# Kernel tuning notes

Measured on AMD Instinct MI355X. Metric: run time of the kernel, lower is better.

The kernel has to match this reference:

```python
import jax, jax.numpy as jnp
import numpy as np

N_NODES = 100000
N_EDGES = 1600000
FEATS = 128
HIDDEN = 64
N_CLASS = 40
NEG_SLOPE = 0.01  # torch leaky_relu default


def _glorot(key, shape):
    lim = float(np.sqrt(6.0 / (shape[0] + shape[1])))
    return jax.random.uniform(key, shape, jnp.float32, -lim, lim)


def setup_inputs() -> dict:
    key = jax.random.key(0)
    ks = jax.random.split(key, 10)
    x = jax.random.normal(ks[0], (N_NODES, FEATS), jnp.float32)
    edge_index = jax.random.randint(ks[1], (2, N_EDGES), 0, N_NODES, jnp.int64)
    edge_weight = jax.random.uniform(ks[2], (N_EDGES,), jnp.float32)
    return {
        "x": x,
        "edge_index": edge_index,
        "edge_weight": edge_weight,
        "W_first": _glorot(ks[3], (FEATS, HIDDEN)),
        "b_first": jnp.zeros((HIDDEN,), jnp.float32),
        "Wc1": _glorot(ks[4], (HIDDEN, HIDDEN)),
        "bc1": jnp.zeros((HIDDEN,), jnp.float32),
        "Wc2": _glorot(ks[5], (HIDDEN, HIDDEN)),
        "bc2": jnp.zeros((HIDDEN,), jnp.float32),
        "W_out": _glorot(ks[6], (HIDDEN, N_CLASS)),
        "b_out": jnp.zeros((N_CLASS,), jnp.float32),
    }


def _gcn_norm(edge_index, edge_weight, n):
    # PyG gcn_norm with add_self_loops=True: A_hat = D^-1/2 (A + I) D^-1/2
    loop = jnp.arange(n, dtype=edge_index.dtype)
    src = jnp.concatenate([edge_index[0], loop])
    dst = jnp.concatenate([edge_index[1], loop])
    ew = jnp.concatenate([edge_weight, jnp.ones((n,), edge_weight.dtype)])
    deg = jax.ops.segment_sum(ew, dst, num_segments=n)  # degree at target
    dis = jnp.where(deg > 0, jax.lax.rsqrt(deg), 0.0)
    norm = dis[src] * ew * dis[dst]  # [E+N]
    return src, dst, norm


def _gcn_conv(h, src, dst, norm, W, b, n):
    h = h @ W                                   # [N, H]
    msg = norm[:, None] * h[src]                # gather + scale  [E+N, H]
    out = jax.ops.segment_sum(msg, dst, num_segments=n)  # scatter-add
    return out + b


def reference(x, edge_index, edge_weight, W_first, b_first, Wc1, bc1, Wc2, bc2, W_out, b_out):
    n = x.shape[0]
    src, dst, norm = _gcn_norm(edge_index, edge_weight, n)
    h = jax.nn.leaky_relu(x @ W_first + b_first, NEG_SLOPE)
    # dropout is identity in eval mode
    h = jax.nn.leaky_relu(_gcn_conv(h, src, dst, norm, Wc1, bc1, n), NEG_SLOPE)
    h = jax.nn.leaky_relu(_gcn_conv(h, src, dst, norm, Wc2, bc2, n), NEG_SLOPE)
    logits = h @ W_out + b_out
    return jax.nn.log_softmax(logits, axis=-1)
```

## Files before the change

kernel.cpp:

```cpp
#include <hip/hip_runtime.h>
#include <hip/hip_bf16.h>
#include <math.h>

#define NFEATS 128
#define NHID   64
#define NCLS   40
#define NEG_SLOPE 0.01f

#define GSH_S  9
#define GSPAN_S 512
#define GCAP_S 9216
#define SB     2048

typedef float f32x4 __attribute__((ext_vector_type(4)));
typedef int   i32x2 __attribute__((ext_vector_type(2)));

__device__ inline unsigned short f2bfu(float v) {
    union { float f; unsigned int u; } x; x.f = v;
    unsigned int r = (x.u + 0x7FFFu + ((x.u >> 16) & 1u)) >> 16;
    return (unsigned short)r;
}
__device__ inline float bf2f(unsigned short u) {
    union { unsigned int u32; float f; } x; x.u32 = ((unsigned int)u) << 16;
    return x.f;
}
__device__ inline float bflo(unsigned int u) {
    union { unsigned int v; float f; } x; x.v = u << 16; return x.f;
}
__device__ inline float bfhi(unsigned int u) {
    union { unsigned int v; float f; } x; x.v = u & 0xFFFF0000u; return x.f;
}

__device__ inline void role_split(int i, int nA, int nB, int* ia, int* ib) {
    *ia = -1; *ib = -1;
    int m2 = 2 * min(nA, nB);
    if (i < m2) { if (i & 1) *ib = i >> 1; else *ia = i >> 1; }
    else if (nA > nB) *ia = i - nB;
    else *ib = i - nA;
}


__global__ __launch_bounds__(256) void stage_gemm1_kernel(
    const int* __restrict__ srcA, const int* __restrict__ dstA, const float* __restrict__ ew,
    int* __restrict__ gcur, int2* __restrict__ staged, int E, int nStage, int ngrp,
    const float* __restrict__ x, const float* __restrict__ W1, const float* __restrict__ b1,
    float* __restrict__ h1, int n, int nTile) {
    __shared__ __align__(16) float Ws[64 * 64];

    int ia, ib;
    role_split(blockIdx.x, nStage, nTile, &ia, &ib);
    int tid = threadIdx.x;

    if (ia >= 0) {
        int* hist = (int*)Ws;
        int* wcur = ((int*)Ws) + 256;
        if (tid < 256) hist[tid] = 0;
        __syncthreads();

        int q0 = (ia * SB) >> 2;
        int qend = min(q0 + SB / 4, E >> 2);
        int dcache[8], scache[8];
        float wcache[8];

#pragma unroll
        for (int it = 0; it < 2; ++it) {
            int q = q0 + it * 256 + tid;
            bool ok = (q < qend);
            int4 d4 = ok ? ((const int4*)dstA)[q] : make_int4(-1, -1, -1, -1);
            int4 s4 = ok ? ((const int4*)srcA)[q] : make_int4(0, 0, 0, 0);
            float4 w4 = ok ? ((const float4*)ew)[q] : make_float4(0, 0, 0, 0);
            dcache[it * 4 + 0] = d4.x; dcache[it * 4 + 1] = d4.y;
            dcache[it * 4 + 2] = d4.z; dcache[it * 4 + 3] = d4.w;
            scache[it * 4 + 0] = s4.x; scache[it * 4 + 1] = s4.y;
            scache[it * 4 + 2] = s4.z; scache[it * 4 + 3] = s4.w;
            wcache[it * 4 + 0] = w4.x; wcache[it * 4 + 1] = w4.y;
            wcache[it * 4 + 2] = w4.z; wcache[it * 4 + 3] = w4.w;
#pragma unroll
            for (int j = 0; j < 4; ++j)
                if (dcache[it * 4 + j] >= 0) atomicAdd(&hist[dcache[it * 4 + j] >> GSH_S], 1);
        }
        if (ia == nStage - 1) {
            for (int e = (E & ~3) + tid; e < E; e += 256) atomicAdd(&hist[dstA[e] >> GSH_S], 1);
        }
        __syncthreads();

        if (tid < ngrp) {
            int c = hist[tid];
            wcur[tid] = (c > 0) ? atomicAdd(&gcur[tid], c) : 0;
        }
        __syncthreads();

        int pos[8];
#pragma unroll
        for (int j = 0; j < 8; ++j) {
            int d = dcache[j];
            pos[j] = (d >= 0) ? atomicAdd(&wcur[d >> GSH_S], 1) : GCAP_S;
        }
#pragma unroll
        for (int j = 0; j < 8; ++j) {
            int d = dcache[j];
            if (d >= 0 && pos[j] < GCAP_S)
                staged[(size_t)(d >> GSH_S) * GCAP_S + pos[j]] =
                    make_int2(((d & (GSPAN_S - 1)) << 17) | scache[j], __float_as_int(wcache[j]));
        }
        if (ia == nStage - 1) {
            for (int e = (E & ~3) + tid; e < E; e += 256) {
                int d = dstA[e];
                int g = d >> GSH_S;
                int p = atomicAdd(&wcur[g], 1);
                if (p < GCAP_S)
                    staged[(size_t)g * GCAP_S + p] =
                        make_int2(((d & (GSPAN_S - 1)) << 17) | srcA[e], __float_as_int(ew[e]));
            }
        }
        return;
    }

    int c4 = (tid & 15) * 4;
    int r0 = ib * 64 + (tid >> 4) * 4;
    int rr[4];
#pragma unroll
    for (int i = 0; i < 4; ++i) rr[i] = min(r0 + i, n - 1);

    float acc[4][4] = {};
    for (int ph = 0; ph < 2; ++ph) {
        __syncthreads();
        for (int i = tid; i < 64 * 16; i += 256)
            ((float4*)Ws)[i] = ((const float4*)W1)[ph * 1024 + i];
        __syncthreads();
#pragma unroll 2
        for (int kk = 0; kk < 64; kk += 4) {
            f32x4 av[4], bv[4];
#pragma unroll
            for (int i = 0; i < 4; ++i)
                av[i] = __builtin_nontemporal_load(
                    (const f32x4*)&x[(size_t)rr[i] * NFEATS + ph * 64 + kk]);
#pragma unroll
            for (int q = 0; q < 4; ++q) bv[q] = *(const f32x4*)&Ws[(kk + q) * 64 + c4];
#pragma unroll
            for (int i = 0; i < 4; ++i) {
#pragma unroll
                for (int q = 0; q < 4; ++q) {
                    float a = av[i][q];
#pragma unroll
                    for (int j = 0; j < 4; ++j) acc[i][j] += a * bv[q][j];
                }
            }
        }
    }

#pragma unroll
    for (int i = 0; i < 4; ++i) {
        int rw = r0 + i;
        if (rw >= n) break;
        float4 o;
        float* oa = (float*)&o;
#pragma unroll
        for (int j = 0; j < 4; ++j) {
            float v = acc[i][j] + b1[c4 + j];
            oa[j] = (v > 0.0f) ? v : v * NEG_SLOPE;
        }
        *(float4*)&h1[(size_t)rw * 64 + c4] = o;
    }
}


__global__ __launch_bounds__(512) void degsort_kernel(
    const int* __restrict__ gcur, const int2* __restrict__ staged,
    int2* __restrict__ staged2, float* __restrict__ dis,
    int2* __restrict__ nodeptr, int n) {
    __shared__ float deg[GSPAN_S];
    __shared__ int hist[GSPAN_S], base[GSPAN_S], cur[GSPAN_S];

    int tid = threadIdx.x;
    int g = blockIdx.x;
    deg[tid] = 0.0f;
    hist[tid] = 0;
    __syncthreads();

    int cnt = min(gcur[g], GCAP_S);
    const int2* sl = staged + (size_t)g * GCAP_S;
    for (int i = tid; i < cnt; i += 512) {
        int2 r = sl[i];
        int dl = r.x >> 17;
        atomicAdd(&deg[dl], __int_as_float(r.y));
        atomicAdd(&hist[dl], 1);
    }
    __syncthreads();

    int node = g * GSPAN_S + tid;
    if (node < n) dis[node] = rsqrtf(1.0f + deg[tid]);

    base[tid] = hist[tid];
    __syncthreads();
    for (int off = 1; off < GSPAN_S; off <<= 1) {
        int t_ = (tid >= off) ? base[tid - off] : 0;
        __syncthreads();
        base[tid] += t_;
        __syncthreads();
    }
    int ex = base[tid] - hist[tid];
    base[tid] = ex;
    cur[tid] = ex;
    __syncthreads();

    if (node < n) nodeptr[node] = make_int2(g * GCAP_S + ex, hist[tid]);

    int2* out = staged2 + (size_t)g * GCAP_S;
    for (int i = tid; i < cnt; i += 512) {
        int2 r = sl[i];
        int dl = r.x >> 17;
        int pos = atomicAdd(&cur[dl], 1);
        out[pos] = make_int2(r.x & 0x1FFFF, r.y);
    }
}


__global__ __launch_bounds__(256) void gemm2s_kernel(
    const float* __restrict__ in, const float* __restrict__ W, const float* __restrict__ dis,
    unsigned short* __restrict__ outp, int n) {
    __shared__ __align__(16) float Ws[NHID * 64];
    int tid = threadIdx.x;
    for (int i = tid; i < NHID * 16; i += 256) ((float4*)Ws)[i] = ((const float4*)W)[i];
    __syncthreads();

    int c4 = (tid & 15) * 4;
    int r0 = blockIdx.x * 64 + (tid >> 4) * 4;
    int rr[4];
#pragma unroll
    for (int i = 0; i < 4; ++i) rr[i] = min(r0 + i, n - 1);

    float acc[4][4] = {};
#pragma unroll 2
    for (int kk = 0; kk < NHID; kk += 4) {
        f32x4 av[4], bv[4];
#pragma unroll
        for (int i = 0; i < 4; ++i)
            av[i] = __builtin_nontemporal_load((const f32x4*)&in[(size_t)rr[i] * NHID + kk]);
#pragma unroll
        for (int q = 0; q < 4; ++q) bv[q] = *(const f32x4*)&Ws[(kk + q) * 64 + c4];
#pragma unroll
        for (int i = 0; i < 4; ++i) {
#pragma unroll
            for (int q = 0; q < 4; ++q) {
                float a = av[i][q];
#pragma unroll
                for (int j = 0; j < 4; ++j) acc[i][j] += a * bv[q][j];
            }
        }
    }

#pragma unroll
    for (int i = 0; i < 4; ++i) {
        int rw = r0 + i;
        if (rw >= n) break;
        float dr = dis[rw];
        ushort4 o;
        o.x = f2bfu(dr * acc[i][0]); o.y = f2bfu(dr * acc[i][1]);
        o.z = f2bfu(dr * acc[i][2]); o.w = f2bfu(dr * acc[i][3]);
        *(ushort4*)&outp[(size_t)rw * 64 + c4] = o;
    }
}


template <int LAYER>
__global__ __launch_bounds__(256) void agg_kernel(const int2* __restrict__ nodeptr,
                                                  const int2* __restrict__ recs0,
                                                  const unsigned short* __restrict__ tb,
                                                  const float* __restrict__ dis,
                                                  const float* __restrict__ bias,
                                                  unsigned short* __restrict__ outp, int n) {
    int wv = threadIdx.x >> 6;
    int lane = threadIdx.x & 63;
    int node = blockIdx.x * 4 + wv;
    if (node >= n) return;

    int2 np = nodeptr[node];
    int start = np.x, c = np.y;
    int grp = lane >> 4;
    int r16 = lane & 15;
    float di = dis[node];

    f32x4 a0 = {0, 0, 0, 0}, a1 = {0, 0, 0, 0}, a2 = {0, 0, 0, 0}, a3 = {0, 0, 0, 0};

    if (grp == 0) {
        uint2 uv = *(const uint2*)&tb[(size_t)node * NHID + r16 * 4];
        a0[0] += bflo(uv.x); a0[1] += bfhi(uv.x);
        a0[2] += bflo(uv.y); a0[3] += bfhi(uv.y);
    }

    const i32x2* recs = (const i32x2*)(recs0 + start);
    for (int b = 0; b < c; b += 64) {
        int rem = min(64, c - b);
        i32x2 ent = (lane < rem) ? recs[b + lane] : (i32x2){0, 0};
        for (int k = 0; k < rem; k += 16) {
            int e0 = k + grp, e1 = k + 4 + grp, e2 = k + 8 + grp, e3 = k + 12 + grp;
            int s0 = __shfl(ent[0], e0); float w0 = __int_as_float(__shfl(ent[1], e0));
            int s1 = __shfl(ent[0], e1); float w1 = __int_as_float(__shfl(ent[1], e1));
            int s2 = __shfl(ent[0], e2); float w2 = __int_as_float(__shfl(ent[1], e2));
            int s3 = __shfl(ent[0], e3); float w3 = __int_as_float(__shfl(ent[1], e3));
            uint2 u0 = *(const uint2*)&tb[(size_t)s0 * NHID + r16 * 4];
            uint2 u1 = *(const uint2*)&tb[(size_t)s1 * NHID + r16 * 4];
            uint2 u2 = *(const uint2*)&tb[(size_t)s2 * NHID + r16 * 4];
            uint2 u3 = *(const uint2*)&tb[(size_t)s3 * NHID + r16 * 4];
            a0[0] += w0 * bflo(u0.x); a0[1] += w0 * bfhi(u0.x);
            a0[2] += w0 * bflo(u0.y); a0[3] += w0 * bfhi(u0.y);
            a1[0] += w1 * bflo(u1.x); a1[1] += w1 * bfhi(u1.x);
            a1[2] += w1 * bflo(u1.y); a1[3] += w1 * bfhi(u1.y);
            a2[0] += w2 * bflo(u2.x); a2[1] += w2 * bfhi(u2.x);
            a2[2] += w2 * bflo(u2.y); a2[3] += w2 * bfhi(u2.y);
            a3[0] += w3 * bflo(u3.x); a3[1] += w3 * bfhi(u3.x);
            a3[2] += w3 * bflo(u3.y); a3[3] += w3 * bfhi(u3.y);
        }
    }

    f32x4 acc;
#pragma unroll
    for (int j = 0; j < 4; ++j) acc[j] = (a0[j] + a1[j]) + (a2[j] + a3[j]);
#pragma unroll
    for (int j = 0; j < 4; ++j) {
        acc[j] += __shfl_xor(acc[j], 16);
        acc[j] += __shfl_xor(acc[j], 32);
    }

    if (lane < 16) {
        ushort4 o;
        unsigned short* op = (unsigned short*)&o;
#pragma unroll
        for (int j = 0; j < 4; ++j) {
            float v;
            if (LAYER == 1) {
                v = di * acc[j] + bias[r16 * 4 + j];
                v = (v > 0.0f) ? v : v * NEG_SLOPE;
                v *= di;
            } else {
                v = di * acc[j];
            }
            op[j] = f2bfu(v);
        }
        *(ushort4*)&outp[(size_t)node * NHID + r16 * 4] = o;
    }
}


__global__ __launch_bounds__(256) void tail_kernel(const unsigned short* __restrict__ ub,
                                                   const float* __restrict__ Wc2,
                                                   const float* __restrict__ bc2,
                                                   const float* __restrict__ Wo,
                                                   const float* __restrict__ bo,
                                                   float* __restrict__ outp, int n) {
    __shared__ __align__(16) float WsA[NHID * 64];
    __shared__ __align__(16) unsigned short hs[64 * 68];
    __shared__ float bos[NCLS];

    int tid = threadIdx.x;
    for (int i = tid; i < NHID * 16; i += 256) ((float4*)WsA)[i] = ((const float4*)Wc2)[i];
    __syncthreads();

    int c4 = (tid & 15) * 4;
    int r0l = (tid >> 4) * 4;
    int base = blockIdx.x * 64;

    int rr[4];
#pragma unroll
    for (int i = 0; i < 4; ++i) rr[i] = min(base + r0l + i, n - 1);

    float acc[4][4] = {};
#pragma unroll 2
    for (int kk = 0; kk < NHID; kk += 4) {
        f32x4 av[4], bv[4];
#pragma unroll
        for (int i = 0; i < 4; ++i) {
            ushort4 uv = *(const ushort4*)&ub[(size_t)rr[i] * NHID + kk];
            av[i][0] = bf2f(uv.x); av[i][1] = bf2f(uv.y);
            av[i][2] = bf2f(uv.z); av[i][3] = bf2f(uv.w);
        }
#pragma unroll
        for (int q = 0; q < 4; ++q) bv[q] = *(const f32x4*)&WsA[(kk + q) * 64 + c4];
#pragma unroll
        for (int i = 0; i < 4; ++i) {
#pragma unroll
            for (int q = 0; q < 4; ++q) {
                float a = av[i][q];
#pragma unroll
                for (int j = 0; j < 4; ++j) acc[i][j] += a * bv[q][j];
            }
        }
    }

#pragma unroll
    for (int i = 0; i < 4; ++i) {
#pragma unroll
        for (int j = 0; j < 4; ++j) {
            float v = acc[i][j] + bc2[c4 + j];
            v = (v > 0.0f) ? v : v * NEG_SLOPE;
            hs[(r0l + i) * 68 + c4 + j] = f2bfu(v);
        }
    }
    __syncthreads();

    for (int i = tid; i < NHID * NCLS / 4; i += 256) ((float4*)WsA)[i] = ((const float4*)Wo)[i];
    if (tid < NCLS) bos[tid] = bo[tid];
    __syncthreads();

    int row = tid >> 2;
    int c0 = (tid & 3) * 10;
    int node = base + row;

    float z[10];
#pragma unroll
    for (int j = 0; j < 10; ++j) z[j] = 0.0f;

#pragma unroll 2
    for (int k0 = 0; k0 < NHID; k0 += 4) {
        ushort4 hv = *(const ushort4*)&hs[row * 68 + k0];
        float h0 = bf2f(hv.x), h1 = bf2f(hv.y), h2 = bf2f(hv.z), h3 = bf2f(hv.w);
        const float* w0 = &WsA[(k0 + 0) * NCLS + c0];
        const float* w1 = &WsA[(k0 + 1) * NCLS + c0];
        const float* w2 = &WsA[(k0 + 2) * NCLS + c0];
        const float* w3 = &WsA[(k0 + 3) * NCLS + c0];
#pragma unroll
        for (int j = 0; j < 10; ++j)
            z[j] += h0 * w0[j] + h1 * w1[j] + h2 * w2[j] + h3 * w3[j];
    }
#pragma unroll
    for (int j = 0; j < 10; ++j) z[j] += bos[c0 + j];

    float m = z[0];
#pragma unroll
    for (int j = 1; j < 10; ++j) m = fmaxf(m, z[j]);
    m = fmaxf(m, __shfl_xor(m, 1));
    m = fmaxf(m, __shfl_xor(m, 2));

    float s = 0.0f;
#pragma unroll
    for (int j = 0; j < 10; ++j) s += expf(z[j] - m);
    s += __shfl_xor(s, 1);
    s += __shfl_xor(s, 2);
    float ls = logf(s);

    if (node < n) {
#pragma unroll
        for (int j = 0; j < 10; ++j)
            outp[(size_t)node * NCLS + c0 + j] = z[j] - m - ls;
    }
}


extern "C" void kernel_launch(void* const* d_in, const int* in_sizes, int n_in,
                              void* d_out, int out_size, void* d_ws, size_t ws_size,
                              hipStream_t stream) {
    const float* x   = (const float*)d_in[0];
    const int*   ei  = (const int*)d_in[1];
    const float* ew  = (const float*)d_in[2];
    const float* W1  = (const float*)d_in[3];
    const float* b1  = (const float*)d_in[4];
    const float* Wc1 = (const float*)d_in[5];
    const float* bc1 = (const float*)d_in[6];
    const float* Wc2 = (const float*)d_in[7];
    const float* bc2 = (const float*)d_in[8];
    const float* Wo  = (const float*)d_in[9];
    const float* bo  = (const float*)d_in[10];
    float* out = (float*)d_out;

    const int N = in_sizes[0] / NFEATS;
    const int E = in_sizes[1] / 2;
    const int* src = ei;
    const int* dst = ei + E;

    const int ngrp   = (N + GSPAN_S - 1) >> GSH_S;
    const int nStage = (E + SB - 1) / SB;
    const int nTile  = (N + 63) / 64;
    const int aggBlocks = (N + 3) / 4;

    float*          bufA  = (float*)d_ws;
    unsigned short* t1b   = (unsigned short*)(bufA + (size_t)N * NHID);
    unsigned short* h2b   = t1b + (size_t)N * NHID;
    int2*  staged  = (int2*)(h2b + (size_t)N * NHID);
    int2*  staged2 = staged + (size_t)ngrp * GCAP_S;
    float* dis     = (float*)(staged2 + (size_t)ngrp * GCAP_S);
    int*   gcur    = (int*)(dis + N);
    int2*  nodeptr = (int2*)(gcur + ((ngrp + 1) & ~1));

    hipMemsetAsync(gcur, 0, ngrp * sizeof(int), stream);

    stage_gemm1_kernel<<<nStage + nTile, 256, 0, stream>>>(
        src, dst, ew, gcur, staged, E, nStage, ngrp, x, W1, b1, bufA, N, nTile);

    degsort_kernel<<<ngrp, 512, 0, stream>>>(gcur, staged, staged2, dis, nodeptr, N);

    gemm2s_kernel<<<nTile, 256, 0, stream>>>(bufA, Wc1, dis, t1b, N);

    agg_kernel<1><<<aggBlocks, 256, 0, stream>>>(nodeptr, staged2, t1b, dis, bc1, h2b, N);

    agg_kernel<2><<<aggBlocks, 256, 0, stream>>>(nodeptr, staged2, h2b, dis, nullptr, t1b, N);

    tail_kernel<<<nTile, 256, 0, stream>>>(t1b, Wc2, bc2, Wo, bo, out, N);
}
```

Baseline: 240.8 us.

## Split degree-sort per group into four quarter blocks for more parallelism

The degree/counting-sort kernel now launches four blocks per 512-node destination group. Each block handles a 128-node quarter and writes into its own output region sized by a new per-quarter capacity. This raises block count (about 196 to about 784) to fill more CUs. The cost is that every block reads the whole group's staged edges, so reads are redundant four times over. The fixed quarter capacity could overflow if a quarter receives more than its share of edges.

```diff
diff --git a/kernel.cpp b/kernel.cpp
--- a/kernel.cpp
+++ b/kernel.cpp
@@ -11,6 +11,7 @@
 #define GSPAN_S 512
 #define GCAP_S 9216
 #define SB     2048
+#define GCAP_Q 2816
 
 typedef float f32x4 __attribute__((ext_vector_type(4)));
 typedef int   i32x2 __attribute__((ext_vector_type(2)));
@@ -165,53 +166,61 @@
 }
 
 
-__global__ __launch_bounds__(512) void degsort_kernel(
+__global__ __launch_bounds__(256) void degsort_kernel(
     const int* __restrict__ gcur, const int2* __restrict__ staged,
     int2* __restrict__ staged2, float* __restrict__ dis,
     int2* __restrict__ nodeptr, int n) {
-    __shared__ float deg[GSPAN_S];
-    __shared__ int hist[GSPAN_S], base[GSPAN_S], cur[GSPAN_S];
+    __shared__ float deg[128];
+    __shared__ int hist[128], basearr[128], cur[128];
 
     int tid = threadIdx.x;
-    int g = blockIdx.x;
-    deg[tid] = 0.0f;
-    hist[tid] = 0;
+    int g = blockIdx.x >> 2;
+    int qtr = blockIdx.x & 3;
+
+    if (tid < 128) { deg[tid] = 0.0f; hist[tid] = 0; }
     __syncthreads();
 
     int cnt = min(gcur[g], GCAP_S);
     const int2* sl = staged + (size_t)g * GCAP_S;
-    for (int i = tid; i < cnt; i += 512) {
+
+    for (int i = tid; i < cnt; i += 256) {
         int2 r = sl[i];
         int dl = r.x >> 17;
-        atomicAdd(&deg[dl], __int_as_float(r.y));
-        atomicAdd(&hist[dl], 1);
-    }
-    __syncthreads();
-
-    int node = g * GSPAN_S + tid;
-    if (node < n) dis[node] = rsqrtf(1.0f + deg[tid]);
-
-    base[tid] = hist[tid];
-    __syncthreads();
-    for (int off = 1; off < GSPAN_S; off <<= 1) {
-        int t_ = (tid >= off) ? base[tid - off] : 0;
-        __syncthreads();
-        base[tid] += t_;
-        __syncthreads();
-    }
-    int ex = base[tid] - hist[tid];
-    base[tid] = ex;
-    cur[tid] = ex;
-    __syncthreads();
-
-    if (node < n) nodeptr[node] = make_int2(g * GCAP_S + ex, hist[tid]);
-
-    int2* out = staged2 + (size_t)g * GCAP_S;
-    for (int i = tid; i < cnt; i += 512) {
+        if ((dl >> 7) == qtr) {
+            atomicAdd(&deg[dl & 127], __int_as_float(r.y));
+            atomicAdd(&hist[dl & 127], 1);
+        }
+    }
+    __syncthreads();
+
+    int node = g * GSPAN_S + qtr * 128 + tid;
+    if (tid < 128 && node < n) dis[node] = rsqrtf(1.0f + deg[tid]);
+
+    if (tid < 128) basearr[tid] = hist[tid];
+    __syncthreads();
+    for (int off = 1; off < 128; off <<= 1) {
+        int t_ = 0;
+        if (tid < 128 && tid >= off) t_ = basearr[tid - off];
+        __syncthreads();
+        if (tid < 128) basearr[tid] += t_;
+        __syncthreads();
+    }
+    int qbase = blockIdx.x * GCAP_Q;
+    if (tid < 128) {
+        int ex = basearr[tid] - hist[tid];
+        cur[tid] = ex;
+        if (node < n) nodeptr[node] = make_int2(qbase + ex, hist[tid]);
+    }
+    __syncthreads();
+
+    int2* out = staged2 + qbase;
+    for (int i = tid; i < cnt; i += 256) {
         int2 r = sl[i];
         int dl = r.x >> 17;
-        int pos = atomicAdd(&cur[dl], 1);
-        out[pos] = make_int2(r.x & 0x1FFFF, r.y);
+        if ((dl >> 7) == qtr) {
+            int pos = atomicAdd(&cur[dl & 127], 1);
+            out[pos] = make_int2(r.x & 0x1FFFF, r.y);
+        }
     }
 }
 
@@ -469,6 +478,7 @@
     const int* dst = ei + E;
 
     const int ngrp   = (N + GSPAN_S - 1) >> GSH_S;
+    const int nSort  = ngrp * 4;
     const int nStage = (E + SB - 1) / SB;
     const int nTile  = (N + 63) / 64;
     const int aggBlocks = (N + 3) / 4;
@@ -478,7 +488,7 @@
     unsigned short* h2b   = t1b + (size_t)N * NHID;
     int2*  staged  = (int2*)(h2b + (size_t)N * NHID);
     int2*  staged2 = staged + (size_t)ngrp * GCAP_S;
-    float* dis     = (float*)(staged2 + (size_t)ngrp * GCAP_S);
+    float* dis     = (float*)(staged2 + (size_t)nSort * GCAP_Q);
     int*   gcur    = (int*)(dis + N);
     int2*  nodeptr = (int2*)(gcur + ((ngrp + 1) & ~1));
 
@@ -487,7 +497,7 @@
     stage_gemm1_kernel<<<nStage + nTile, 256, 0, stream>>>(
         src, dst, ew, gcur, staged, E, nStage, ngrp, x, W1, b1, bufA, N, nTile);
 
-    degsort_kernel<<<ngrp, 512, 0, stream>>>(gcur, staged, staged2, dis, nodeptr, N);
+    degsort_kernel<<<nSort, 256, 0, stream>>>(gcur, staged, staged2, dis, nodeptr, N);
 
     gemm2s_kernel<<<nTile, 256, 0, stream>>>(bufA, Wc1, dis, t1b, N);
 
```

New measurement: 254.9 us. 1.06x slower.
